# Kernel optimization log

Measured on AMD Instinct MI355X. Metric: run time of the kernel, lower is better.

The kernel has to match this reference:

```python
import jax, jax.numpy as jnp
import numpy as np
import math

HIDDEN = 1024
HEADS = 16
HEAD_DIM = HIDDEN // HEADS
B, S = 2, 2048


def _xavier(key, shape):
    fan_in, fan_out = shape[1], shape[0]
    limit = math.sqrt(6.0 / (fan_in + fan_out))
    return jax.random.uniform(key, shape, jnp.float32, -limit, limit)


def setup_inputs() -> dict:
    key = jax.random.key(0)
    ks = jax.random.split(key, 5)
    x = jax.random.normal(ks[0], (B, S, HIDDEN), jnp.float32)
    # torch Linear stores weight as [out, in]; y = x @ W.T + b
    Wq = _xavier(ks[1], (HIDDEN, HIDDEN))
    Wk = _xavier(ks[2], (HIDDEN, HIDDEN))
    Wv = _xavier(ks[3], (HIDDEN, HIDDEN))
    Wo = _xavier(ks[4], (HIDDEN, HIDDEN))
    bq = jnp.zeros((HIDDEN,), jnp.float32)
    bk = jnp.zeros((HIDDEN,), jnp.float32)
    bv = jnp.zeros((HIDDEN,), jnp.float32)
    bo = jnp.zeros((HIDDEN,), jnp.float32)
    return {"x": x, "Wq": Wq, "bq": bq, "Wk": Wk, "bk": bk,
            "Wv": Wv, "bv": bv, "Wo": Wo, "bo": bo}


def reference(x, Wq, bq, Wk, bk, Wv, bv, Wo, bo):
    b, s, d = x.shape
    h, hd = HEADS, HEAD_DIM
    q = (x @ Wq.T + bq).reshape(b, s, h, hd).transpose(0, 2, 1, 3)  # [b,h,s,hd]
    k = (x @ Wk.T + bk).reshape(b, s, h, hd).transpose(0, 2, 1, 3)
    v = (x @ Wv.T + bv).reshape(b, s, h, hd).transpose(0, 2, 1, 3)
    scores = jnp.einsum('bhqd,bhkd->bhqk', q, k) / math.sqrt(hd)
    causal = jnp.tril(jnp.ones((s, s), bool))
    scores = jnp.where(causal, scores, -jnp.inf)
    attn = jax.nn.softmax(scores, axis=-1)
    out = jnp.einsum('bhqk,bhkd->bhqd', attn, v)  # [b,h,s,hd]
    out = out.transpose(0, 2, 1, 3).reshape(b, s, d)
    return out @ Wo.T + bo
```

## Files before the change

### kernel.cpp

```cpp
#include <hip/hip_runtime.h>
#include <hip/hip_bf16.h>


typedef __hip_bfloat16 bf16;
typedef __attribute__((ext_vector_type(8))) short short8;
typedef __attribute__((ext_vector_type(4))) short short4v;
typedef __attribute__((ext_vector_type(4))) float f32x4;

#define MFMA16(a, b, c) __builtin_amdgcn_mfma_f32_16x16x32_bf16((a), (b), (c), 0, 0, 0)

__device__ __forceinline__ void load_lds16(const void* g, void* l) {
  __builtin_amdgcn_global_load_lds(
      (const __attribute__((address_space(1))) void*)g,
      (__attribute__((address_space(3))) void*)l, 16, 0, 0);
}

#define QSCALE 0.18033688f

__global__ __launch_bounds__(256) void cvt_kernel(
    const float* __restrict__ x, const float* __restrict__ wq,
    const float* __restrict__ wk, const float* __restrict__ wv,
    const float* __restrict__ wo, bf16* __restrict__ xb,
    bf16* __restrict__ wcat) {
  const int bx = blockIdx.x;
  const float* src;
  bf16* dst;
  int ib;
  if (bx < 4096) { src = x; dst = xb; ib = bx; }
  else {
    const int wseg = (bx - 4096) >> 10;
    ib = (bx - 4096) & 1023;
    src = wseg == 0 ? wq : wseg == 1 ? wk : wseg == 2 ? wv : wo;
    dst = wcat + (size_t)wseg * 1048576;
  }
  const int i = (ib * 256 + threadIdx.x) * 4;
  const float4 v = *(const float4*)(src + i);
  short4v p;
  *(__hip_bfloat162*)&p = __float22bfloat162_rn(float2{v.x, v.y});
  *((__hip_bfloat162*)&p + 1) = __float22bfloat162_rn(float2{v.z, v.w});
  *(short4v*)(dst + i) = p;
}

__global__ __launch_bounds__(256) void qkv_kernel(
    const bf16* __restrict__ x, const bf16* __restrict__ Wcat,
    const float* __restrict__ bq, const float* __restrict__ bk,
    const float* __restrict__ bv, bf16* __restrict__ Qb,
    bf16* __restrict__ Kb, bf16* __restrict__ Vtg) {
  constexpr int K = 1024;
  __shared__ bf16 As[128 * 64];
  __shared__ bf16 Bs[128 * 64];
  const int t = threadIdx.x;
  const int lane = t & 63, w = t >> 6;
  const int quad = lane >> 4, r = lane & 15;
  const int m0 = blockIdx.y * 128;
  const int ncol = blockIdx.x * 128;
  const int seg = ncol >> 10;
  const int n0 = ncol & 1023;
  const int wm = w >> 1, wn = w & 1;

  f32x4 acc[4][4] = {};

  for (int k0 = 0; k0 < K; k0 += 64) {
    __syncthreads();
#pragma unroll
    for (int p = 0; p < 4; ++p) {
      const int c = p * 256 + w * 64 + lane;
      const int row = c >> 3;
      const int scb = (c & 7) ^ (row & 7);
      load_lds16(x + (size_t)(m0 + row) * K + k0 + scb * 8, As + c * 8);
    }
#pragma unroll
    for (int p = 0; p < 4; ++p) {
      const int c = p * 256 + w * 64 + lane;
      const int row = c >> 3;
      const int scb = (c & 7) ^ (row & 7);
      load_lds16(Wcat + (size_t)(ncol + row) * K + k0 + scb * 8, Bs + c * 8);
    }
    __syncthreads();
    short8 af[4][2], bfr[4][2];
#pragma unroll
    for (int ks = 0; ks < 2; ++ks) {
#pragma unroll
      for (int i = 0; i < 4; ++i) {
        const int ra = wm * 64 + i * 16 + r;
        af[i][ks] = *(const short8*)(As + ra * 64 +
                                     (((ks * 4 + quad) ^ (ra & 7)) * 8));
        const int rb = wn * 64 + i * 16 + r;
        bfr[i][ks] = *(const short8*)(Bs + rb * 64 +
                                      (((ks * 4 + quad) ^ (rb & 7)) * 8));
      }
    }
#pragma unroll
    for (int ks = 0; ks < 2; ++ks)
#pragma unroll
      for (int i = 0; i < 4; ++i)
#pragma unroll
        for (int j = 0; j < 4; ++j)
          acc[i][j] = MFMA16(af[i][ks], bfr[j][ks], acc[i][j]);
  }

  const float* bias = seg == 0 ? bq : seg == 1 ? bk : bv;
  const float scale = seg == 0 ? QSCALE : 1.0f;
  bf16* dst01 = seg == 0 ? Qb : Kb;
#pragma unroll
  for (int i = 0; i < 4; ++i) {
    const int m = m0 + wm * 64 + i * 16 + quad * 4;
#pragma unroll
    for (int j = 0; j < 4; ++j) {
      const int nn = n0 + wn * 64 + j * 16 + r;
      const float bv_ = bias[nn];
      if (seg == 2) {
        short4v pk;
        *(__hip_bfloat162*)&pk = __float22bfloat162_rn(
            float2{acc[i][j][0] + bv_, acc[i][j][1] + bv_});
        *((__hip_bfloat162*)&pk + 1) = __float22bfloat162_rn(
            float2{acc[i][j][2] + bv_, acc[i][j][3] + bv_});
        *(short4v*)(Vtg + (size_t)nn * 4096 + m) = pk;
      } else {
#pragma unroll
        for (int g = 0; g < 4; ++g)
          dst01[(size_t)(m + g) * 1024 + nn] =
              __float2bfloat16((acc[i][j][g] + bv_) * scale);
      }
    }
  }
}

__global__ __launch_bounds__(256) void proj_kernel(const bf16* __restrict__ X,
                                                   const bf16* __restrict__ W,
                                                   const float* __restrict__ bias,
                                                   float* __restrict__ Y) {
  constexpr int K = 1024, N = 1024;
  __shared__ bf16 As[64 * 64];
  __shared__ bf16 Bs[128 * 64];
  const int t = threadIdx.x;
  const int lane = t & 63, w = t >> 6;
  const int quad = lane >> 4, r = lane & 15;
  const int m0 = blockIdx.y * 64, n0 = blockIdx.x * 128;
  const int wm = w >> 1, wn = w & 1;

  f32x4 acc[2][4] = {};

  for (int k0 = 0; k0 < K; k0 += 64) {
    __syncthreads();
#pragma unroll
    for (int p = 0; p < 2; ++p) {
      const int c = p * 256 + w * 64 + lane;
      const int row = c >> 3;
      const int scb = (c & 7) ^ (row & 7);
      load_lds16(X + (size_t)(m0 + row) * K + k0 + scb * 8, As + c * 8);
    }
#pragma unroll
    for (int p = 0; p < 4; ++p) {
      const int c = p * 256 + w * 64 + lane;
      const int row = c >> 3;
      const int scb = (c & 7) ^ (row & 7);
      load_lds16(W + (size_t)(n0 + row) * K + k0 + scb * 8, Bs + c * 8);
    }
    __syncthreads();
    short8 af[2][2], bfr[4][2];
#pragma unroll
    for (int ks = 0; ks < 2; ++ks) {
#pragma unroll
      for (int i = 0; i < 2; ++i) {
        const int ra = wm * 32 + i * 16 + r;
        af[i][ks] = *(const short8*)(As + ra * 64 +
                                     (((ks * 4 + quad) ^ (ra & 7)) * 8));
      }
#pragma unroll
      for (int j = 0; j < 4; ++j) {
        const int rb = wn * 64 + j * 16 + r;
        bfr[j][ks] = *(const short8*)(Bs + rb * 64 +
                                      (((ks * 4 + quad) ^ (rb & 7)) * 8));
      }
    }
#pragma unroll
    for (int ks = 0; ks < 2; ++ks)
#pragma unroll
      for (int i = 0; i < 2; ++i)
#pragma unroll
        for (int j = 0; j < 4; ++j)
          acc[i][j] = MFMA16(af[i][ks], bfr[j][ks], acc[i][j]);
  }
#pragma unroll
  for (int i = 0; i < 2; ++i) {
    const int m = m0 + wm * 32 + i * 16 + quad * 4;
#pragma unroll
    for (int j = 0; j < 4; ++j) {
      const int n = n0 + wn * 64 + j * 16 + r;
      const float bv = bias[n];
#pragma unroll
      for (int g = 0; g < 4; ++g)
        Y[(size_t)(m + g) * N + n] = acc[i][j][g] + bv;
    }
  }
}

__global__ __launch_bounds__(256) void attn_kernel(const bf16* __restrict__ Qb,
                                                   const bf16* __restrict__ Kb,
                                                   const bf16* __restrict__ Vtg,
                                                   bf16* __restrict__ Ob) {
  const int pair = blockIdx.x, h = blockIdx.y, b = blockIdx.z;
  const int t = threadIdx.x;
  const int lane = t & 63, w = t >> 6;
  const int quad = lane >> 4, r = lane & 15;

  __shared__ bf16 Ks[128 * 64];
  __shared__ bf16 Vt[64 * 128];
  __shared__ bf16 Pl[4][2][16 * 128];

  const bf16 *kp[4], *vp[4];
  bf16 *klds[4], *vlds[4];
#pragma unroll
  for (int p = 0; p < 4; ++p) {
    const int c = p * 256 + w * 64 + lane;
    const int rowK = c >> 3, scbK = (c & 7) ^ (rowK & 7);
    const int rowV = c >> 4, scbV = (c & 15) ^ (rowV & 15);
    klds[p] = Ks + c * 8;
    vlds[p] = Vt + c * 8;
    kp[p] = Kb + (size_t)(b * 2048 + rowK) * 1024 + h * 64 + scbK * 8;
    vp[p] = Vtg + (size_t)(h * 64 + rowV) * 4096 + b * 2048 + scbV * 8;
  }

  const int jlo = pair, jhi = 31 - pair;
  const int nkt_lo = jlo / 2 + 1, nkt_hi = jhi / 2 + 1;
  const int qrow_lo = jlo * 64 + w * 16 + r;
  const int qrow_hi = jhi * 64 + w * 16 + r;

  short8 qfl[2], qfh[2];
#pragma unroll
  for (int ks = 0; ks < 2; ++ks) {
    qfl[ks] = *(const short8*)(Qb + (size_t)(b * 2048 + qrow_lo) * 1024 +
                               h * 64 + ks * 32 + quad * 8);
    qfh[ks] = *(const short8*)(Qb + (size_t)(b * 2048 + qrow_hi) * 1024 +
                               h * 64 + ks * 32 + quad * 8);
  }

  f32x4 oh[4] = {}, ol[4] = {};
  float lsh = 0.f, lsl = 0.f;

  for (int kt = 0; kt < nkt_hi; ++kt) {
    const int k0 = kt * 128;
    __syncthreads();
#pragma unroll
    for (int p = 0; p < 4; ++p) load_lds16(kp[p], klds[p]);
#pragma unroll
    for (int p = 0; p < 4; ++p) load_lds16(vp[p], vlds[p]);
#pragma unroll
    for (int p = 0; p < 4; ++p) { kp[p] += 128 * 1024; vp[p] += 128; }
    __syncthreads();

    const bool lo_act = (kt < nkt_lo);

    auto s_phase = [&](const short8* qf, int qrow, bool mask, int qi,
                       float& lsum) {
      f32x4 st[8] = {};
#pragma unroll
      for (int ks = 0; ks < 2; ++ks) {
        short8 kf[8];
#pragma unroll
        for (int mt = 0; mt < 8; ++mt) {
          const int key = mt * 16 + r;
          kf[mt] = *(const short8*)(Ks + key * 64 +
                                    (((ks * 4 + quad) ^ (key & 7)) * 8));
        }
#pragma unroll
        for (int mt = 0; mt < 8; ++mt) st[mt] = MFMA16(kf[mt], qf[ks], st[mt]);
      }
      if (mask) {
#pragma unroll
        for (int mt = 0; mt < 8; ++mt)
#pragma unroll
          for (int g = 0; g < 4; ++g) {
            const int key = k0 + mt * 16 + quad * 4 + g;
            if (key > qrow) st[mt][g] = -1e30f;
          }
      }
#pragma unroll
      for (int mt = 0; mt < 8; ++mt) {
        const float p0 = exp2f(st[mt][0]), p1 = exp2f(st[mt][1]);
        const float p2 = exp2f(st[mt][2]), p3 = exp2f(st[mt][3]);
        lsum += (p0 + p1) + (p2 + p3);
        short4v pk;
        *(__hip_bfloat162*)&pk = __float22bfloat162_rn(float2{p0, p1});
        *((__hip_bfloat162*)&pk + 1) = __float22bfloat162_rn(float2{p2, p3});
        const int key8 = mt * 2 + (quad >> 1);
        const int off = r * 128 + ((key8 ^ (r & 15)) * 8) + (quad & 1) * 4;
        *(short4v*)(&Pl[w][qi][off]) = pk;
      }
    };

    s_phase(qfh, qrow_hi, kt == nkt_hi - 1, 0, lsh);
    if (lo_act) s_phase(qfl, qrow_lo, kt == nkt_lo - 1, 1, lsl);

    asm volatile("s_waitcnt lgkmcnt(0)" ::: "memory");

#pragma unroll
    for (int ks = 0; ks < 4; ++ks) {
      short8 vf[4];
#pragma unroll
      for (int mt = 0; mt < 4; ++mt) {
        const int d = mt * 16 + r;
        vf[mt] = *(const short8*)(Vt + d * 128 +
                                  (((ks * 4 + quad) ^ (d & 15)) * 8));
      }
      const int poff = r * 128 + (((ks * 4 + quad) ^ (r & 15)) * 8);
      const short8 pfh = *(const short8*)(Pl[w][0] + poff);
#pragma unroll
      for (int mt = 0; mt < 4; ++mt) oh[mt] = MFMA16(vf[mt], pfh, oh[mt]);
      if (lo_act) {
        const short8 pfl = *(const short8*)(Pl[w][1] + poff);
#pragma unroll
        for (int mt = 0; mt < 4; ++mt) ol[mt] = MFMA16(vf[mt], pfl, ol[mt]);
      }
    }
  }

  lsh += __shfl_xor(lsh, 16);
  lsh += __shfl_xor(lsh, 32);
  lsl += __shfl_xor(lsl, 16);
  lsl += __shfl_xor(lsl, 32);
  const float invh = 1.f / lsh, invl = 1.f / lsl;

#pragma unroll
  for (int mt = 0; mt < 4; ++mt) {
    const int d0 = mt * 16 + quad * 4;
    short4v ph, pl2;
    *(__hip_bfloat162*)&ph = __float22bfloat162_rn(
        float2{oh[mt][0] * invh, oh[mt][1] * invh});
    *((__hip_bfloat162*)&ph + 1) = __float22bfloat162_rn(
        float2{oh[mt][2] * invh, oh[mt][3] * invh});
    *(short4v*)(Ob + (size_t)(b * 2048 + qrow_hi) * 1024 + h * 64 + d0) = ph;
    *(__hip_bfloat162*)&pl2 = __float22bfloat162_rn(
        float2{ol[mt][0] * invl, ol[mt][1] * invl});
    *((__hip_bfloat162*)&pl2 + 1) = __float22bfloat162_rn(
        float2{ol[mt][2] * invl, ol[mt][3] * invl});
    *(short4v*)(Ob + (size_t)(b * 2048 + qrow_lo) * 1024 + h * 64 + d0) = pl2;
  }
}

extern "C" void kernel_launch(void* const* d_in, const int* in_sizes, int n_in,
                              void* d_out, int out_size, void* d_ws, size_t ws_size,
                              hipStream_t stream) {
  const float* x  = (const float*)d_in[0];
  const float* Wq = (const float*)d_in[1];
  const float* bq = (const float*)d_in[2];
  const float* Wk = (const float*)d_in[3];
  const float* bk = (const float*)d_in[4];
  const float* Wv = (const float*)d_in[5];
  const float* bv = (const float*)d_in[6];
  const float* Wo = (const float*)d_in[7];
  const float* bo = (const float*)d_in[8];
  float* out = (float*)d_out;

  bf16* xb   = (bf16*)d_ws;
  bf16* wcat = xb + (size_t)4096 * 1024;
  bf16* wob  = wcat + (size_t)3 * 1024 * 1024;
  bf16* Qb   = wcat + (size_t)4 * 1024 * 1024;
  bf16* Kb   = Qb  + (size_t)4096 * 1024;
  bf16* Vtg  = Kb  + (size_t)4096 * 1024;
  bf16* Ob   = Vtg + (size_t)4096 * 1024;
  const size_t need = ((size_t)4096 * 1024 * 5 + (size_t)1024 * 1024 * 4) * 2;
  if (ws_size < need) return;

  cvt_kernel<<<8192, 256, 0, stream>>>(x, Wq, Wk, Wv, Wo, xb, wcat);
  qkv_kernel<<<dim3(24, 32), 256, 0, stream>>>(xb, wcat, bq, bk, bv,
                                               Qb, Kb, Vtg);
  attn_kernel<<<dim3(16, 16, 2), 256, 0, stream>>>(Qb, Kb, Vtg, Ob);
  proj_kernel<<<dim3(8, 64), 256, 0, stream>>>(Ob, wob, bo, out);
}
```

Before: 189.2 us.

## Split attention into one q-tile per block with double-buffered 64-key K/V tiles

The attention kernel stops pairing a low and a high query tile per block and launches one 64-row query tile per block, with the heaviest tiles scheduled first. Key tiles shrink from 128 to 64 and K/V are double-buffered in LDS, so the next tile's global-to-LDS load is issued before the current one is computed. Launch bounds request 4 blocks per CU to raise occupancy. The aim is to hide load latency and balance the causal workload, at the cost of more blocks, more barriers per key, and losing the pairing's built-in load balance.

```diff
diff --git a/kernel.cpp b/kernel.cpp
--- a/kernel.cpp
+++ b/kernel.cpp
@@ -196,146 +196,135 @@
   }
 }
 
-__global__ __launch_bounds__(256) void attn_kernel(const bf16* __restrict__ Qb,
-                                                   const bf16* __restrict__ Kb,
-                                                   const bf16* __restrict__ Vtg,
-                                                   bf16* __restrict__ Ob) {
-  const int pair = blockIdx.x, h = blockIdx.y, b = blockIdx.z;
+__global__ __launch_bounds__(256, 4) void attn_kernel(const bf16* __restrict__ Qb,
+                                                      const bf16* __restrict__ Kb,
+                                                      const bf16* __restrict__ Vtg,
+                                                      bf16* __restrict__ Ob) {
+  const int j = 31 - blockIdx.x;
+  const int h = blockIdx.y, b = blockIdx.z;
   const int t = threadIdx.x;
   const int lane = t & 63, w = t >> 6;
   const int quad = lane >> 4, r = lane & 15;
 
-  __shared__ bf16 Ks[128 * 64];
-  __shared__ bf16 Vt[64 * 128];
-  __shared__ bf16 Pl[4][2][16 * 128];
-
-  const bf16 *kp[4], *vp[4];
-  bf16 *klds[4], *vlds[4];
-#pragma unroll
-  for (int p = 0; p < 4; ++p) {
-    const int c = p * 256 + w * 64 + lane;
-    const int rowK = c >> 3, scbK = (c & 7) ^ (rowK & 7);
-    const int rowV = c >> 4, scbV = (c & 15) ^ (rowV & 15);
-    klds[p] = Ks + c * 8;
-    vlds[p] = Vt + c * 8;
-    kp[p] = Kb + (size_t)(b * 2048 + rowK) * 1024 + h * 64 + scbK * 8;
-    vp[p] = Vtg + (size_t)(h * 64 + rowV) * 4096 + b * 2048 + scbV * 8;
-  }
-
-  const int jlo = pair, jhi = 31 - pair;
-  const int nkt_lo = jlo / 2 + 1, nkt_hi = jhi / 2 + 1;
-  const int qrow_lo = jlo * 64 + w * 16 + r;
-  const int qrow_hi = jhi * 64 + w * 16 + r;
-
-  short8 qfl[2], qfh[2];
-#pragma unroll
-  for (int ks = 0; ks < 2; ++ks) {
-    qfl[ks] = *(const short8*)(Qb + (size_t)(b * 2048 + qrow_lo) * 1024 +
-                               h * 64 + ks * 32 + quad * 8);
-    qfh[ks] = *(const short8*)(Qb + (size_t)(b * 2048 + qrow_hi) * 1024 +
-                               h * 64 + ks * 32 + quad * 8);
-  }
-
-  f32x4 oh[4] = {}, ol[4] = {};
-  float lsh = 0.f, lsl = 0.f;
-
-  for (int kt = 0; kt < nkt_hi; ++kt) {
-    const int k0 = kt * 128;
-    __syncthreads();
-#pragma unroll
-    for (int p = 0; p < 4; ++p) load_lds16(kp[p], klds[p]);
-#pragma unroll
-    for (int p = 0; p < 4; ++p) load_lds16(vp[p], vlds[p]);
-#pragma unroll
-    for (int p = 0; p < 4; ++p) { kp[p] += 128 * 1024; vp[p] += 128; }
-    __syncthreads();
-
-    const bool lo_act = (kt < nkt_lo);
-
-    auto s_phase = [&](const short8* qf, int qrow, bool mask, int qi,
-                       float& lsum) {
-      f32x4 st[8] = {};
-#pragma unroll
-      for (int ks = 0; ks < 2; ++ks) {
-        short8 kf[8];
-#pragma unroll
-        for (int mt = 0; mt < 8; ++mt) {
-          const int key = mt * 16 + r;
-          kf[mt] = *(const short8*)(Ks + key * 64 +
-                                    (((ks * 4 + quad) ^ (key & 7)) * 8));
+  __shared__ bf16 Ks[2][64 * 64];
+  __shared__ bf16 Vt[2][64 * 64];
+  __shared__ bf16 Pl[4][16 * 64];
+
+  const int nkt = j + 1;
+  const int qrow = j * 64 + w * 16 + r;
+
+  short8 qf[2];
+#pragma unroll
+  for (int ks = 0; ks < 2; ++ks)
+    qf[ks] = *(const short8*)(Qb + (size_t)(b * 2048 + qrow) * 1024 +
+                              h * 64 + ks * 32 + quad * 8);
+
+  const bf16 *kg[2], *vg[2];
+  int lofs[2];
+#pragma unroll
+  for (int p = 0; p < 2; ++p) {
+    const int c = p * 256 + t;
+    const int row = c >> 3, scb = (c & 7) ^ (row & 7);
+    kg[p] = Kb + (size_t)(b * 2048 + row) * 1024 + h * 64 + scb * 8;
+    vg[p] = Vtg + (size_t)(h * 64 + row) * 4096 + b * 2048 + scb * 8;
+    lofs[p] = c * 8;
+  }
+
+  auto stage = [&](int kt, int bs) {
+#pragma unroll
+    for (int p = 0; p < 2; ++p)
+      load_lds16(kg[p] + (size_t)kt * 65536, &Ks[bs][lofs[p]]);
+#pragma unroll
+    for (int p = 0; p < 2; ++p)
+      load_lds16(vg[p] + (size_t)kt * 64, &Vt[bs][lofs[p]]);
+  };
+
+  f32x4 o[4] = {};
+  float lsum = 0.f;
+  bf16* const plw = Pl[w];
+
+  auto compute = [&](int kt, int bs, bool mask) {
+    const bf16* const ksb = Ks[bs];
+    const bf16* const vtb = Vt[bs];
+    f32x4 st[4] = {};
+#pragma unroll
+    for (int ks = 0; ks < 2; ++ks) {
+      short8 kf[4];
+#pragma unroll
+      for (int mt = 0; mt < 4; ++mt) {
+        const int key = mt * 16 + r;
+        kf[mt] = *(const short8*)(ksb + key * 64 +
+                                  (((ks * 4 + quad) ^ (key & 7)) * 8));
+      }
+#pragma unroll
+      for (int mt = 0; mt < 4; ++mt) st[mt] = MFMA16(kf[mt], qf[ks], st[mt]);
+    }
+    if (mask) {
+#pragma unroll
+      for (int mt = 0; mt < 4; ++mt)
+#pragma unroll
+        for (int g = 0; g < 4; ++g) {
+          const int key = kt * 64 + mt * 16 + quad * 4 + g;
+          if (key > qrow) st[mt][g] = -1e30f;
         }
-#pragma unroll
-        for (int mt = 0; mt < 8; ++mt) st[mt] = MFMA16(kf[mt], qf[ks], st[mt]);
-      }
-      if (mask) {
-#pragma unroll
-        for (int mt = 0; mt < 8; ++mt)
-#pragma unroll
-          for (int g = 0; g < 4; ++g) {
-            const int key = k0 + mt * 16 + quad * 4 + g;
-            if (key > qrow) st[mt][g] = -1e30f;
-          }
-      }
-#pragma unroll
-      for (int mt = 0; mt < 8; ++mt) {
-        const float p0 = exp2f(st[mt][0]), p1 = exp2f(st[mt][1]);
-        const float p2 = exp2f(st[mt][2]), p3 = exp2f(st[mt][3]);
-        lsum += (p0 + p1) + (p2 + p3);
-        short4v pk;
-        *(__hip_bfloat162*)&pk = __float22bfloat162_rn(float2{p0, p1});
-        *((__hip_bfloat162*)&pk + 1) = __float22bfloat162_rn(float2{p2, p3});
-        const int key8 = mt * 2 + (quad >> 1);
-        const int off = r * 128 + ((key8 ^ (r & 15)) * 8) + (quad & 1) * 4;
-        *(short4v*)(&Pl[w][qi][off]) = pk;
-      }
-    };
-
-    s_phase(qfh, qrow_hi, kt == nkt_hi - 1, 0, lsh);
-    if (lo_act) s_phase(qfl, qrow_lo, kt == nkt_lo - 1, 1, lsl);
-
+    }
+#pragma unroll
+    for (int mt = 0; mt < 4; ++mt) {
+      const float p0 = exp2f(st[mt][0]), p1 = exp2f(st[mt][1]);
+      const float p2 = exp2f(st[mt][2]), p3 = exp2f(st[mt][3]);
+      lsum += (p0 + p1) + (p2 + p3);
+      short4v pk;
+      *(__hip_bfloat162*)&pk = __float22bfloat162_rn(float2{p0, p1});
+      *((__hip_bfloat162*)&pk + 1) = __float22bfloat162_rn(float2{p2, p3});
+      const int key8 = mt * 2 + (quad >> 1);
+      *(short4v*)(plw + r * 64 + ((key8 ^ (r & 7)) * 8) + (quad & 1) * 4) = pk;
+    }
     asm volatile("s_waitcnt lgkmcnt(0)" ::: "memory");
-
-#pragma unroll
-    for (int ks = 0; ks < 4; ++ks) {
+#pragma unroll
+    for (int ks = 0; ks < 2; ++ks) {
       short8 vf[4];
 #pragma unroll
       for (int mt = 0; mt < 4; ++mt) {
         const int d = mt * 16 + r;
-        vf[mt] = *(const short8*)(Vt + d * 128 +
-                                  (((ks * 4 + quad) ^ (d & 15)) * 8));
-      }
-      const int poff = r * 128 + (((ks * 4 + quad) ^ (r & 15)) * 8);
-      const short8 pfh = *(const short8*)(Pl[w][0] + poff);
-#pragma unroll
-      for (int mt = 0; mt < 4; ++mt) oh[mt] = MFMA16(vf[mt], pfh, oh[mt]);
-      if (lo_act) {
-        const short8 pfl = *(const short8*)(Pl[w][1] + poff);
-#pragma unroll
-        for (int mt = 0; mt < 4; ++mt) ol[mt] = MFMA16(vf[mt], pfl, ol[mt]);
-      }
-    }
-  }
-
-  lsh += __shfl_xor(lsh, 16);
-  lsh += __shfl_xor(lsh, 32);
-  lsl += __shfl_xor(lsl, 16);
-  lsl += __shfl_xor(lsl, 32);
-  const float invh = 1.f / lsh, invl = 1.f / lsl;
+        vf[mt] = *(const short8*)(vtb + d * 64 +
+                                  (((ks * 4 + quad) ^ (d & 7)) * 8));
+      }
+      const short8 pf =
+          *(const short8*)(plw + r * 64 + (((ks * 4 + quad) ^ (r & 7)) * 8));
+#pragma unroll
+      for (int mt = 0; mt < 4; ++mt) o[mt] = MFMA16(vf[mt], pf, o[mt]);
+    }
+  };
+
+  stage(0, 0);
+  int kt = 0;
+  for (; kt < nkt - 1; ++kt) {
+    stage(kt + 1, (kt + 1) & 1);
+    asm volatile("s_waitcnt vmcnt(4)" ::: "memory");
+    __builtin_amdgcn_s_barrier();
+    __builtin_amdgcn_sched_barrier(0);
+    compute(kt, kt & 1, false);
+    __builtin_amdgcn_sched_barrier(0);
+    __builtin_amdgcn_s_barrier();
+  }
+  asm volatile("s_waitcnt vmcnt(0)" ::: "memory");
+  __builtin_amdgcn_s_barrier();
+  __builtin_amdgcn_sched_barrier(0);
+  compute(kt, kt & 1, true);
+
+  lsum += __shfl_xor(lsum, 16);
+  lsum += __shfl_xor(lsum, 32);
+  const float inv = 1.f / lsum;
 
 #pragma unroll
   for (int mt = 0; mt < 4; ++mt) {
     const int d0 = mt * 16 + quad * 4;
-    short4v ph, pl2;
+    short4v ph;
     *(__hip_bfloat162*)&ph = __float22bfloat162_rn(
-        float2{oh[mt][0] * invh, oh[mt][1] * invh});
+        float2{o[mt][0] * inv, o[mt][1] * inv});
     *((__hip_bfloat162*)&ph + 1) = __float22bfloat162_rn(
-        float2{oh[mt][2] * invh, oh[mt][3] * invh});
-    *(short4v*)(Ob + (size_t)(b * 2048 + qrow_hi) * 1024 + h * 64 + d0) = ph;
-    *(__hip_bfloat162*)&pl2 = __float22bfloat162_rn(
-        float2{ol[mt][0] * invl, ol[mt][1] * invl});
-    *((__hip_bfloat162*)&pl2 + 1) = __float22bfloat162_rn(
-        float2{ol[mt][2] * invl, ol[mt][3] * invl});
-    *(short4v*)(Ob + (size_t)(b * 2048 + qrow_lo) * 1024 + h * 64 + d0) = pl2;
+        float2{o[mt][2] * inv, o[mt][3] * inv});
+    *(short4v*)(Ob + (size_t)(b * 2048 + qrow) * 1024 + h * 64 + d0) = ph;
   }
 }
 
@@ -366,6 +355,6 @@
   cvt_kernel<<<8192, 256, 0, stream>>>(x, Wq, Wk, Wv, Wo, xb, wcat);
   qkv_kernel<<<dim3(24, 32), 256, 0, stream>>>(xb, wcat, bq, bk, bv,
                                                Qb, Kb, Vtg);
-  attn_kernel<<<dim3(16, 16, 2), 256, 0, stream>>>(Qb, Kb, Vtg, Ob);
+  attn_kernel<<<dim3(32, 16, 2), 256, 0, stream>>>(Qb, Kb, Vtg, Ob);
   proj_kernel<<<dim3(8, 64), 256, 0, stream>>>(Ob, wob, bo, out);
 }
```

Result: slower. 201.7 us (+6.6%).

## Split attention key tiles across two wave groups with double-buffered async staging

Applied to the files above, without the earlier changes.

Rewrites the attention kernel to use 512-thread blocks in which two groups of four waves each handle alternate 64-key tiles. K/V tiles are double-buffered through async global-to-LDS loads with explicit vmcnt waits, so the next tiles load while the current ones are computed. Partial outputs and row sums from the two groups are combined through LDS at the end. Block indices are also remapped so that neighbouring blocks share heads, which may help cache locality. The costs are an extra reduction step, more registers per thread under the launch bounds, and two barriers per iteration.

```diff
diff --git a/kernel.cpp b/kernel.cpp
--- a/kernel.cpp
+++ b/kernel.cpp
@@ -196,146 +196,206 @@
   }
 }
 
-__global__ __launch_bounds__(256) void attn_kernel(const bf16* __restrict__ Qb,
-                                                   const bf16* __restrict__ Kb,
-                                                   const bf16* __restrict__ Vtg,
-                                                   bf16* __restrict__ Ob) {
-  const int pair = blockIdx.x, h = blockIdx.y, b = blockIdx.z;
+__global__ __launch_bounds__(512, 4) void attn_kernel(const bf16* __restrict__ Qb,
+                                                      const bf16* __restrict__ Kb,
+                                                      const bf16* __restrict__ Vtg,
+                                                      bf16* __restrict__ Ob) {
+  const int n = blockIdx.x;
+  const int gl = n & 7, pair = (n >> 3) & 15, gh = n >> 7;
+  const int g = gl + 8 * gh;
+  const int h = g & 15, b = g >> 4;
   const int t = threadIdx.x;
   const int lane = t & 63, w = t >> 6;
+  const int grp = w >> 2, ww = w & 3;
   const int quad = lane >> 4, r = lane & 15;
 
-  __shared__ bf16 Ks[128 * 64];
-  __shared__ bf16 Vt[64 * 128];
-  __shared__ bf16 Pl[4][2][16 * 128];
-
-  const bf16 *kp[4], *vp[4];
-  bf16 *klds[4], *vlds[4];
-#pragma unroll
-  for (int p = 0; p < 4; ++p) {
-    const int c = p * 256 + w * 64 + lane;
-    const int rowK = c >> 3, scbK = (c & 7) ^ (rowK & 7);
-    const int rowV = c >> 4, scbV = (c & 15) ^ (rowV & 15);
-    klds[p] = Ks + c * 8;
-    vlds[p] = Vt + c * 8;
-    kp[p] = Kb + (size_t)(b * 2048 + rowK) * 1024 + h * 64 + scbK * 8;
-    vp[p] = Vtg + (size_t)(h * 64 + rowV) * 4096 + b * 2048 + scbV * 8;
-  }
+  __shared__ __align__(16) bf16 Ks[2][2][64 * 64];
+  __shared__ __align__(16) bf16 Vt[2][2][64 * 64];
+  __shared__ __align__(16) bf16 Pl[8][16 * 64];
 
   const int jlo = pair, jhi = 31 - pair;
-  const int nkt_lo = jlo / 2 + 1, nkt_hi = jhi / 2 + 1;
-  const int qrow_lo = jlo * 64 + w * 16 + r;
-  const int qrow_hi = jhi * 64 + w * 16 + r;
-
-  short8 qfl[2], qfh[2];
+  const int NL = jlo + 1, T = jhi + 1;
+  const int nit = (T + 1) >> 1;
+  const int qrow_lo = jlo * 64 + ww * 16 + r;
+  const int qrow_hi = jhi * 64 + ww * 16 + r;
+
+  short8 qfh[2], qfl[2];
 #pragma unroll
   for (int ks = 0; ks < 2; ++ks) {
+    qfh[ks] = *(const short8*)(Qb + (size_t)(b * 2048 + qrow_hi) * 1024 +
+                               h * 64 + ks * 32 + quad * 8);
     qfl[ks] = *(const short8*)(Qb + (size_t)(b * 2048 + qrow_lo) * 1024 +
                                h * 64 + ks * 32 + quad * 8);
-    qfh[ks] = *(const short8*)(Qb + (size_t)(b * 2048 + qrow_hi) * 1024 +
-                               h * 64 + ks * 32 + quad * 8);
-  }
+  }
+
+  const int c = t;
+  const int row = c >> 3, scb = (c & 7) ^ (row & 7);
+  const bf16* const kg = Kb + (size_t)(b * 2048 + row) * 1024 + h * 64 + scb * 8;
+  const bf16* const vg = Vtg + (size_t)(h * 64 + row) * 4096 +
+                         (size_t)b * 2048 + scb * 8;
+
+  auto stage = [&](int tile, int half, int sub) {
+    load_lds16(kg + (size_t)tile * 65536, &Ks[half][sub][c * 8]);
+    load_lds16(vg + tile * 64, &Vt[half][sub][c * 8]);
+  };
 
   f32x4 oh[4] = {}, ol[4] = {};
   float lsh = 0.f, lsl = 0.f;
-
-  for (int kt = 0; kt < nkt_hi; ++kt) {
-    const int k0 = kt * 128;
-    __syncthreads();
-#pragma unroll
-    for (int p = 0; p < 4; ++p) load_lds16(kp[p], klds[p]);
-#pragma unroll
-    for (int p = 0; p < 4; ++p) load_lds16(vp[p], vlds[p]);
-#pragma unroll
-    for (int p = 0; p < 4; ++p) { kp[p] += 128 * 1024; vp[p] += 128; }
-    __syncthreads();
-
-    const bool lo_act = (kt < nkt_lo);
-
-    auto s_phase = [&](const short8* qf, int qrow, bool mask, int qi,
-                       float& lsum) {
-      f32x4 st[8] = {};
+  bf16* const plw = Pl[w];
+
+  auto compute = [&](int kt, int half, int sub) {
+    const bf16* const ksb = Ks[half][sub];
+    const bf16* const vtb = Vt[half][sub];
+    const bool lo = (kt < NL);
+    f32x4 sh[4] = {}, sl[4] = {};
+#pragma unroll
+    for (int ks = 0; ks < 2; ++ks) {
+      short8 kf[4];
+#pragma unroll
+      for (int mt = 0; mt < 4; ++mt)
+        kf[mt] = *(const short8*)(ksb + (mt * 16 + r) * 64 +
+                                  (((ks * 4 + quad) ^ (r & 7)) * 8));
+#pragma unroll
+      for (int mt = 0; mt < 4; ++mt) sh[mt] = MFMA16(kf[mt], qfh[ks], sh[mt]);
+      if (lo) {
+#pragma unroll
+        for (int mt = 0; mt < 4; ++mt) sl[mt] = MFMA16(kf[mt], qfl[ks], sl[mt]);
+      }
+    }
+    if (kt == T - 1) {
+#pragma unroll
+      for (int mt = 0; mt < 4; ++mt)
+#pragma unroll
+        for (int g4 = 0; g4 < 4; ++g4) {
+          const int key = kt * 64 + mt * 16 + quad * 4 + g4;
+          if (key > qrow_hi) sh[mt][g4] = -1e30f;
+        }
+    }
+#pragma unroll
+    for (int mt = 0; mt < 4; ++mt) {
+      const float p0 = exp2f(sh[mt][0]), p1 = exp2f(sh[mt][1]);
+      const float p2 = exp2f(sh[mt][2]), p3 = exp2f(sh[mt][3]);
+      lsh += (p0 + p1) + (p2 + p3);
+      short4v pk;
+      *(__hip_bfloat162*)&pk = __float22bfloat162_rn(float2{p0, p1});
+      *((__hip_bfloat162*)&pk + 1) = __float22bfloat162_rn(float2{p2, p3});
+      const int key8 = mt * 2 + (quad >> 1);
+      *(short4v*)(plw + r * 64 + ((key8 ^ (r & 7)) * 8) + (quad & 1) * 4) = pk;
+    }
+    short4v pkl[4];
+    if (lo) {
+      if (kt == NL - 1) {
+#pragma unroll
+        for (int mt = 0; mt < 4; ++mt)
+#pragma unroll
+          for (int g4 = 0; g4 < 4; ++g4) {
+            const int key = kt * 64 + mt * 16 + quad * 4 + g4;
+            if (key > qrow_lo) sl[mt][g4] = -1e30f;
+          }
+      }
+#pragma unroll
+      for (int mt = 0; mt < 4; ++mt) {
+        const float p0 = exp2f(sl[mt][0]), p1 = exp2f(sl[mt][1]);
+        const float p2 = exp2f(sl[mt][2]), p3 = exp2f(sl[mt][3]);
+        lsl += (p0 + p1) + (p2 + p3);
+        *(__hip_bfloat162*)&pkl[mt] = __float22bfloat162_rn(float2{p0, p1});
+        *((__hip_bfloat162*)&pkl[mt] + 1) =
+            __float22bfloat162_rn(float2{p2, p3});
+      }
+    }
+    asm volatile("s_waitcnt lgkmcnt(0)" ::: "memory");
+    short8 vf[2][4];
+#pragma unroll
+    for (int ks = 0; ks < 2; ++ks) {
+#pragma unroll
+      for (int mt = 0; mt < 4; ++mt)
+        vf[ks][mt] = *(const short8*)(vtb + (mt * 16 + r) * 64 +
+                                      (((ks * 4 + quad) ^ (r & 7)) * 8));
+      const short8 pf =
+          *(const short8*)(plw + r * 64 + (((ks * 4 + quad) ^ (r & 7)) * 8));
+#pragma unroll
+      for (int mt = 0; mt < 4; ++mt) oh[mt] = MFMA16(vf[ks][mt], pf, oh[mt]);
+    }
+    if (lo) {
+#pragma unroll
+      for (int mt = 0; mt < 4; ++mt) {
+        const int key8 = mt * 2 + (quad >> 1);
+        *(short4v*)(plw + r * 64 + ((key8 ^ (r & 7)) * 8) + (quad & 1) * 4) =
+            pkl[mt];
+      }
+      asm volatile("s_waitcnt lgkmcnt(0)" ::: "memory");
 #pragma unroll
       for (int ks = 0; ks < 2; ++ks) {
-        short8 kf[8];
-#pragma unroll
-        for (int mt = 0; mt < 8; ++mt) {
-          const int key = mt * 16 + r;
-          kf[mt] = *(const short8*)(Ks + key * 64 +
-                                    (((ks * 4 + quad) ^ (key & 7)) * 8));
-        }
-#pragma unroll
-        for (int mt = 0; mt < 8; ++mt) st[mt] = MFMA16(kf[mt], qf[ks], st[mt]);
-      }
-      if (mask) {
-#pragma unroll
-        for (int mt = 0; mt < 8; ++mt)
-#pragma unroll
-          for (int g = 0; g < 4; ++g) {
-            const int key = k0 + mt * 16 + quad * 4 + g;
-            if (key > qrow) st[mt][g] = -1e30f;
-          }
-      }
-#pragma unroll
-      for (int mt = 0; mt < 8; ++mt) {
-        const float p0 = exp2f(st[mt][0]), p1 = exp2f(st[mt][1]);
-        const float p2 = exp2f(st[mt][2]), p3 = exp2f(st[mt][3]);
-        lsum += (p0 + p1) + (p2 + p3);
-        short4v pk;
-        *(__hip_bfloat162*)&pk = __float22bfloat162_rn(float2{p0, p1});
-        *((__hip_bfloat162*)&pk + 1) = __float22bfloat162_rn(float2{p2, p3});
-        const int key8 = mt * 2 + (quad >> 1);
-        const int off = r * 128 + ((key8 ^ (r & 15)) * 8) + (quad & 1) * 4;
-        *(short4v*)(&Pl[w][qi][off]) = pk;
-      }
-    };
-
-    s_phase(qfh, qrow_hi, kt == nkt_hi - 1, 0, lsh);
-    if (lo_act) s_phase(qfl, qrow_lo, kt == nkt_lo - 1, 1, lsl);
-
-    asm volatile("s_waitcnt lgkmcnt(0)" ::: "memory");
-
-#pragma unroll
-    for (int ks = 0; ks < 4; ++ks) {
-      short8 vf[4];
-#pragma unroll
-      for (int mt = 0; mt < 4; ++mt) {
-        const int d = mt * 16 + r;
-        vf[mt] = *(const short8*)(Vt + d * 128 +
-                                  (((ks * 4 + quad) ^ (d & 15)) * 8));
-      }
-      const int poff = r * 128 + (((ks * 4 + quad) ^ (r & 15)) * 8);
-      const short8 pfh = *(const short8*)(Pl[w][0] + poff);
-#pragma unroll
-      for (int mt = 0; mt < 4; ++mt) oh[mt] = MFMA16(vf[mt], pfh, oh[mt]);
-      if (lo_act) {
-        const short8 pfl = *(const short8*)(Pl[w][1] + poff);
-#pragma unroll
-        for (int mt = 0; mt < 4; ++mt) ol[mt] = MFMA16(vf[mt], pfl, ol[mt]);
-      }
-    }
-  }
-
-  lsh += __shfl_xor(lsh, 16);
-  lsh += __shfl_xor(lsh, 32);
-  lsl += __shfl_xor(lsl, 16);
-  lsl += __shfl_xor(lsl, 32);
-  const float invh = 1.f / lsh, invl = 1.f / lsl;
-
-#pragma unroll
-  for (int mt = 0; mt < 4; ++mt) {
-    const int d0 = mt * 16 + quad * 4;
-    short4v ph, pl2;
-    *(__hip_bfloat162*)&ph = __float22bfloat162_rn(
-        float2{oh[mt][0] * invh, oh[mt][1] * invh});
-    *((__hip_bfloat162*)&ph + 1) = __float22bfloat162_rn(
-        float2{oh[mt][2] * invh, oh[mt][3] * invh});
-    *(short4v*)(Ob + (size_t)(b * 2048 + qrow_hi) * 1024 + h * 64 + d0) = ph;
-    *(__hip_bfloat162*)&pl2 = __float22bfloat162_rn(
-        float2{ol[mt][0] * invl, ol[mt][1] * invl});
-    *((__hip_bfloat162*)&pl2 + 1) = __float22bfloat162_rn(
-        float2{ol[mt][2] * invl, ol[mt][3] * invl});
-    *(short4v*)(Ob + (size_t)(b * 2048 + qrow_lo) * 1024 + h * 64 + d0) = pl2;
+        const short8 pf =
+            *(const short8*)(plw + r * 64 + (((ks * 4 + quad) ^ (r & 7)) * 8));
+#pragma unroll
+        for (int mt = 0; mt < 4; ++mt) ol[mt] = MFMA16(vf[ks][mt], pf, ol[mt]);
+      }
+    }
+  };
+
+  stage(0, 0, 0);
+  stage(1, 0, 1);
+  for (int i = 0; i < nit; ++i) {
+    const int half = i & 1, nhalf = half ^ 1;
+    const int t2 = 2 * i + 2, t3 = 2 * i + 3;
+    int nis = 0;
+    if (t2 < T) { stage(t2, nhalf, 0); nis += 2; }
+    if (t3 < T) { stage(t3, nhalf, 1); nis += 2; }
+    if (nis == 4)      asm volatile("s_waitcnt vmcnt(4)" ::: "memory");
+    else if (nis == 2) asm volatile("s_waitcnt vmcnt(2)" ::: "memory");
+    else               asm volatile("s_waitcnt vmcnt(0)" ::: "memory");
+    __builtin_amdgcn_s_barrier();
+    __builtin_amdgcn_sched_barrier(0);
+    const int myt = 2 * i + grp;
+    if (myt < T) compute(myt, half, grp);
+    __builtin_amdgcn_sched_barrier(0);
+    __builtin_amdgcn_s_barrier();
+  }
+
+  __syncthreads();
+  f32x4* const cb = (f32x4*)&Ks[0][0][0];
+  float* const lb = (float*)&Vt[0][0][0];
+  if (grp == 1) {
+#pragma unroll
+    for (int mt = 0; mt < 4; ++mt) {
+      cb[((ww * 2 + 0) * 4 + mt) * 64 + lane] = oh[mt];
+      cb[((ww * 2 + 1) * 4 + mt) * 64 + lane] = ol[mt];
+    }
+    lb[(ww * 2 + 0) * 64 + lane] = lsh;
+    lb[(ww * 2 + 1) * 64 + lane] = lsl;
+  }
+  __syncthreads();
+  if (grp == 0) {
+#pragma unroll
+    for (int mt = 0; mt < 4; ++mt) {
+      const f32x4 ah = cb[((ww * 2 + 0) * 4 + mt) * 64 + lane];
+      const f32x4 al = cb[((ww * 2 + 1) * 4 + mt) * 64 + lane];
+#pragma unroll
+      for (int g4 = 0; g4 < 4; ++g4) { oh[mt][g4] += ah[g4]; ol[mt][g4] += al[g4]; }
+    }
+    lsh += lb[(ww * 2 + 0) * 64 + lane];
+    lsl += lb[(ww * 2 + 1) * 64 + lane];
+    lsh += __shfl_xor(lsh, 16);
+    lsh += __shfl_xor(lsh, 32);
+    lsl += __shfl_xor(lsl, 16);
+    lsl += __shfl_xor(lsl, 32);
+    const float invh = 1.f / lsh, invl = 1.f / lsl;
+#pragma unroll
+    for (int mt = 0; mt < 4; ++mt) {
+      const int d0 = mt * 16 + quad * 4;
+      short4v ph, pl2;
+      *(__hip_bfloat162*)&ph = __float22bfloat162_rn(
+          float2{oh[mt][0] * invh, oh[mt][1] * invh});
+      *((__hip_bfloat162*)&ph + 1) = __float22bfloat162_rn(
+          float2{oh[mt][2] * invh, oh[mt][3] * invh});
+      *(short4v*)(Ob + (size_t)(b * 2048 + qrow_hi) * 1024 + h * 64 + d0) = ph;
+      *(__hip_bfloat162*)&pl2 = __float22bfloat162_rn(
+          float2{ol[mt][0] * invl, ol[mt][1] * invl});
+      *((__hip_bfloat162*)&pl2 + 1) = __float22bfloat162_rn(
+          float2{ol[mt][2] * invl, ol[mt][3] * invl});
+      *(short4v*)(Ob + (size_t)(b * 2048 + qrow_lo) * 1024 + h * 64 + d0) = pl2;
+    }
   }
 }
 
@@ -366,6 +426,6 @@
   cvt_kernel<<<8192, 256, 0, stream>>>(x, Wq, Wk, Wv, Wo, xb, wcat);
   qkv_kernel<<<dim3(24, 32), 256, 0, stream>>>(xb, wcat, bq, bk, bv,
                                                Qb, Kb, Vtg);
-  attn_kernel<<<dim3(16, 16, 2), 256, 0, stream>>>(Qb, Kb, Vtg, Ob);
+  attn_kernel<<<512, 512, 0, stream>>>(Qb, Kb, Vtg, Ob);
   proj_kernel<<<dim3(8, 64), 256, 0, stream>>>(Ob, wob, bo, out);
 }
```

Measured after the change: 182.9 us. 3.3% less time.
